# Kernel tuning notes

Measured on AMD Instinct MI355X. Metric: run time of the kernel, lower is better.

## Reference

```python
import jax, jax.numpy as jnp
import numpy as np
import math

B, TQ, TK, C, H, DFF = 4, 1024, 1024, 1024, 16, 4096
DK = C // H
EPS = 1e-12


def _mha(x_q, x_kv, wq, bq, wk, bk, wv, bv, wo, bo, mask):
    Bq, Tq, Cq = x_q.shape
    Tk = x_kv.shape[1]
    q = (x_q @ wq + bq).reshape(Bq, Tq, H, DK).transpose(0, 2, 1, 3)  # [B,H,Tq,dk]
    k = (x_kv @ wk + bk).reshape(Bq, Tk, H, DK).transpose(0, 2, 1, 3)
    v = (x_kv @ wv + bv).reshape(Bq, Tk, H, DK).transpose(0, 2, 1, 3)
    scores = jnp.einsum('bhqd,bhkd->bhqk', q, k) * (1.0 / math.sqrt(DK))
    if mask is not None:
        scores = jnp.where(mask, scores, jnp.asarray(-1e9, scores.dtype))
    attn = jax.nn.softmax(scores, axis=-1)
    o = jnp.einsum('bhqk,bhkd->bhqd', attn, v).transpose(0, 2, 1, 3).reshape(Bq, Tq, Cq)
    return o @ wo + bo


def _ln(x, g, b):
    mu = jnp.mean(x, axis=-1, keepdims=True)
    var = jnp.mean(jnp.square(x - mu), axis=-1, keepdims=True)
    return (x - mu) * jax.lax.rsqrt(var + EPS) * g + b


def setup_inputs() -> dict:
    key = jax.random.key(0)
    ks = iter(jax.random.split(key, 32))
    s = 0.02
    inp = {}
    inp['src'] = jax.random.normal(next(ks), (B, TK, C), jnp.float32)
    inp['dst'] = jax.random.normal(next(ks), (B, TQ, C), jnp.float32)
    inp['src_mask'] = jnp.ones((B, 1, 1, TK), dtype=bool)  # key-padding mask (all valid)
    inp['dst_mask'] = jnp.tril(jnp.ones((TQ, TQ), dtype=bool))[None, None]  # causal
    for p in ['sa', 'ca']:
        for n in ['wq', 'wk', 'wv', 'wo']:
            inp[f'{p}_{n}'] = jax.random.normal(next(ks), (C, C), jnp.float32) * s
        for n in ['bq', 'bk', 'bv', 'bo']:
            inp[f'{p}_{n}'] = jnp.zeros((C,), jnp.float32)
    inp['ffn_w1'] = jax.random.normal(next(ks), (C, DFF), jnp.float32) * s
    inp['ffn_b1'] = jnp.zeros((DFF,), jnp.float32)
    inp['ffn_w2'] = jax.random.normal(next(ks), (DFF, C), jnp.float32) * s
    inp['ffn_b2'] = jnp.zeros((C,), jnp.float32)
    for i in ['1', '2', '3']:
        inp[f'ln{i}_g'] = jnp.ones((C,), jnp.float32)
        inp[f'ln{i}_b'] = jnp.zeros((C,), jnp.float32)
    return inp


def reference(src, dst, src_mask, dst_mask,
              sa_wq, sa_wk, sa_wv, sa_wo, sa_bq, sa_bk, sa_bv, sa_bo,
              ca_wq, ca_wk, ca_wv, ca_wo, ca_bq, ca_bk, ca_bv, ca_bo,
              ffn_w1, ffn_b1, ffn_w2, ffn_b2,
              ln1_g, ln1_b, ln2_g, ln2_b, ln3_g, ln3_b):
    # post-LN decoder layer, eval mode (dropout is identity)
    sa = _mha(dst, dst, sa_wq, sa_bq, sa_wk, sa_bk, sa_wv, sa_bv, sa_wo, sa_bo, dst_mask)
    y = _ln(dst + sa, ln1_g, ln1_b)
    ca = _mha(y, src, ca_wq, ca_bq, ca_wk, ca_bk, ca_wv, ca_bv, ca_wo, ca_bo, src_mask)
    y = _ln(y + ca, ln2_g, ln2_b)
    ff = jax.nn.gelu(y @ ffn_w1 + ffn_b1, approximate=False) @ ffn_w2 + ffn_b2
    return _ln(y + ff, ln3_g, ln3_b)
```

## Files before the change

### kernel.cpp

```cpp
#include <hip/hip_runtime.h>
#include <math.h>

typedef __attribute__((ext_vector_type(4))) float f32x4;
typedef __attribute__((ext_vector_type(8))) __bf16 bf16x8;
typedef __attribute__((ext_vector_type(8))) short short8;

#define DEV __device__ __forceinline__

DEV short f2bfs(float f) {
    unsigned u = __builtin_bit_cast(unsigned, f);
    unsigned r = (u + 0x7FFFu + ((u >> 16) & 1u)) >> 16;
    return (short)r;
}

DEV f32x4 mfma16(bf16x8 a, bf16x8 b, f32x4 c) {
    return __builtin_amdgcn_mfma_f32_16x16x32_bf16(a, b, c, 0, 0, 0);
}

DEV void gload_lds16(const void* g, void* l) {
    __builtin_amdgcn_global_load_lds((const __attribute__((address_space(1))) void*)g,
                                     (__attribute__((address_space(3))) void*)l, 16, 0, 0);
}

__global__ __launch_bounds__(256) void wtrans(const float* __restrict__ Win,
                                              short* __restrict__ Wout,
                                              int Kd, int Nd) {
    __shared__ float Tt[64][65];
    const int tx = threadIdx.x & 15, ty = threadIdx.x >> 4;
    const int k0 = blockIdx.y * 64, n0 = blockIdx.x * 64;
#pragma unroll
    for (int rr = 0; rr < 4; ++rr) {
        int k = ty + rr * 16;
        float4 v = *(const float4*)&Win[(size_t)(k0 + k) * Nd + n0 + tx * 4];
        Tt[k][tx * 4 + 0] = v.x; Tt[k][tx * 4 + 1] = v.y;
        Tt[k][tx * 4 + 2] = v.z; Tt[k][tx * 4 + 3] = v.w;
    }
    __syncthreads();
#pragma unroll
    for (int rr = 0; rr < 4; ++rr) {
        int n = ty + rr * 16;
        short4 o;
        o.x = f2bfs(Tt[tx * 4 + 0][n]);
        o.y = f2bfs(Tt[tx * 4 + 1][n]);
        o.z = f2bfs(Tt[tx * 4 + 2][n]);
        o.w = f2bfs(Tt[tx * 4 + 3][n]);
        *(short4*)&Wout[(size_t)(n0 + n) * Kd + k0 + tx * 4] = o;
    }
}

struct WPtrs { const float* p[8]; };

__global__ __launch_bounds__(256) void wtrans8(WPtrs wp, short* __restrict__ out) {
    const float* __restrict__ Win = wp.p[blockIdx.z];
    short* __restrict__ Wout = out + (size_t)blockIdx.z * (1024 * 1024);
    __shared__ float Tt[64][65];
    const int tx = threadIdx.x & 15, ty = threadIdx.x >> 4;
    const int k0 = blockIdx.y * 64, n0 = blockIdx.x * 64;
#pragma unroll
    for (int rr = 0; rr < 4; ++rr) {
        int k = ty + rr * 16;
        float4 v = *(const float4*)&Win[(size_t)(k0 + k) * 1024 + n0 + tx * 4];
        Tt[k][tx * 4 + 0] = v.x; Tt[k][tx * 4 + 1] = v.y;
        Tt[k][tx * 4 + 2] = v.z; Tt[k][tx * 4 + 3] = v.w;
    }
    __syncthreads();
#pragma unroll
    for (int rr = 0; rr < 4; ++rr) {
        int n = ty + rr * 16;
        short4 o;
        o.x = f2bfs(Tt[tx * 4 + 0][n]);
        o.y = f2bfs(Tt[tx * 4 + 1][n]);
        o.z = f2bfs(Tt[tx * 4 + 2][n]);
        o.w = f2bfs(Tt[tx * 4 + 3][n]);
        *(short4*)&Wout[(size_t)(n0 + n) * 1024 + k0 + tx * 4] = o;
    }
}

__global__ __launch_bounds__(256) void conv_bf16(const float* __restrict__ X,
                                                 short* __restrict__ Y, int n8) {
    int i = blockIdx.x * 256 + threadIdx.x;
    if (i < n8) {
        float4 a = ((const float4*)X)[i * 2];
        float4 b = ((const float4*)X)[i * 2 + 1];
        short8 o;
        o[0] = f2bfs(a.x); o[1] = f2bfs(a.y); o[2] = f2bfs(a.z); o[3] = f2bfs(a.w);
        o[4] = f2bfs(b.x); o[5] = f2bfs(b.y); o[6] = f2bfs(b.z); o[7] = f2bfs(b.w);
        ((short8*)Y)[i] = o;
    }
}

template <int BM, int BN, int BK, int EPI, bool SWZ>
__global__ __launch_bounds__(256, (BM == 64 && BN == 64) ? 5 : 1)
void gemm_bt(const short* __restrict__ A,
             const short* __restrict__ BT,
             const float* __restrict__ b0,
             const float* __restrict__ b1,
             const float* __restrict__ b2,
             void* __restrict__ o0,
             void* __restrict__ o1,
             void* __restrict__ o2,
             int M, int N, int K, int Ks) {
    constexpr int IM = BM / 32, JN = BN / 32;
    constexpr int KH = BK / 32;
    constexpr int AL = (BM * 64) / 4096;
    constexpr int BL = (BN * 64) / 4096;
    __shared__ __align__(16) short As[2][BM * BK];
    __shared__ __align__(16) short Bs[2][BN * BK];
    const int tid = threadIdx.x, lane = tid & 63, w = tid >> 6;

    int bx, by, bz;
    if (SWZ) {
        int gx = gridDim.x, gy = gridDim.y;
        int G = gx * gy * gridDim.z;
        int fid = blockIdx.x + gx * (blockIdx.y + gy * blockIdx.z);
        int nf = (fid & 7) * (G >> 3) + (fid >> 3);
        bx = nf % gx;
        int t = nf / gx;
        by = t % gy;
        bz = t / gy;
    } else {
        bx = blockIdx.x; by = blockIdx.y; bz = blockIdx.z;
    }

    const int m0 = by * BM, n0 = bx * BN;
    const int kz = bz * K;
    const int wm = (w & 1) * (BM / 2), wn = (w >> 1) * (BN / 2);
    const int rl = lane & 15, rg = lane >> 4;
    f32x4 acc[IM][JN] = {};
    const char* Ab = (const char*)A;
    const char* Bb = (const char*)BT;
    const int nk = K / BK;

    auto stage = [&](int kt, int buf) {
#pragma unroll
        for (int h = 0; h < KH; ++h) {
#pragma unroll
            for (int r = 0; r < AL; ++r) {
                int lo = (tid + r * 256) * 16;
                int row = lo >> 6, cp = (lo >> 4) & 3, c = (cp - (row >> 1)) & 3;
                gload_lds16(Ab + ((size_t)(m0 + row) * Ks + kz + kt * BK + h * 32 + c * 8) * 2,
                            (char*)As[buf] + h * (BM * 64) + lo);
            }
#pragma unroll
            for (int r = 0; r < BL; ++r) {
                int lo = (tid + r * 256) * 16;
                int row = lo >> 6, cp = (lo >> 4) & 3, c = (cp - (row >> 1)) & 3;
                gload_lds16(Bb + ((size_t)(n0 + row) * Ks + kz + kt * BK + h * 32 + c * 8) * 2,
                            (char*)Bs[buf] + h * (BN * 64) + lo);
            }
        }
    };

    stage(0, 0);
    for (int kt = 0; kt < nk; ++kt) {
        const int buf = kt & 1;
        __syncthreads();
        if (kt + 1 < nk) stage(kt + 1, buf ^ 1);
        bf16x8 af[KH][IM], bfr[KH][JN];
#pragma unroll
        for (int h = 0; h < KH; ++h) {
#pragma unroll
            for (int i = 0; i < IM; i++) {
                int row = wm + i * 16 + rl;
                af[h][i] = *(const bf16x8*)(As[buf] + h * (BM * 32) + row * 32 +
                                            ((rg + (row >> 1)) & 3) * 8);
            }
#pragma unroll
            for (int j = 0; j < JN; j++) {
                int row = wn + j * 16 + rl;
                bfr[h][j] = *(const bf16x8*)(Bs[buf] + h * (BN * 32) + row * 32 +
                                             ((rg + (row >> 1)) & 3) * 8);
            }
        }
#pragma unroll
        for (int h = 0; h < KH; ++h)
#pragma unroll
            for (int i = 0; i < IM; i++)
#pragma unroll
                for (int j = 0; j < JN; j++)
                    acc[i][j] = mfma16(af[h][i], bfr[h][j], acc[i][j]);
    }

    float* o0z = (float*)o0 + (size_t)bz * M * N;
#pragma unroll
    for (int i = 0; i < IM; i++) {
        int gm0 = m0 + wm + i * 16 + rg * 4;
#pragma unroll
        for (int j = 0; j < JN; j++) {
            int gn = n0 + wn + j * 16 + rl;
            if (EPI == 0) {
                float bv = bz == 0 ? b0[gn] : 0.0f;
#pragma unroll
                for (int r = 0; r < 4; r++)
                    o0z[(size_t)(gm0 + r) * N + gn] = acc[i][j][r] + bv;
            } else if (EPI == 2) {
                float bv = b0[gn];
#pragma unroll
                for (int r = 0; r < 4; r++) {
                    float x = acc[i][j][r] + bv;
                    float z = 1.59576912f * x + 0.07135481f * x * x * x;
                    float g = x / (1.0f + __expf(-z));
                    ((short*)o0)[(size_t)(gm0 + r) * N + gn] = f2bfs(g);
                }
            } else {
                int seg = gn >> 10, n1 = gn & 1023, h = n1 >> 6, d = n1 & 63;
                int b = gm0 >> 10, t0 = gm0 & 1023;
                bool isV = (EPI == 1) ? (seg == 2) : (seg == 1);
                const float* bp = (EPI == 1) ? (seg == 0 ? b0 : (seg == 1 ? b1 : b2))
                                             : (seg == 0 ? b0 : b1);
                float bv = bp[n1];
                float qs = (EPI == 1 && seg == 0) ? 0.125f : 1.0f;
                if (!isV) {
                    short* hp = (short*)((EPI == 1) ? (seg == 0 ? o0 : o1) : o0);
                    size_t base = ((size_t)(b * 16 + h) * 1024 + t0) * 64 + d;
#pragma unroll
                    for (int r = 0; r < 4; r++)
                        hp[base + (size_t)r * 64] = f2bfs((acc[i][j][r] + bv) * qs);
                } else {
                    short* vp = (short*)((EPI == 1) ? o2 : o1);
                    short4 pk;
                    pk.x = f2bfs(acc[i][j][0] + bv);
                    pk.y = f2bfs(acc[i][j][1] + bv);
                    pk.z = f2bfs(acc[i][j][2] + bv);
                    pk.w = f2bfs(acc[i][j][3] + bv);
                    *(short4*)(vp + ((size_t)(b * 16 + h) * 64 + d) * 1024 + t0) = pk;
                }
            }
        }
    }
}

template <bool CAUSAL>
__global__ __launch_bounds__(256, 3) void attn4(const short* __restrict__ Qh,
                                                const short* __restrict__ Kh,
                                                const short* __restrict__ VTh,
                                                short* __restrict__ Out, int TKn) {
    __shared__ __align__(16) short Ks[2][64 * 64];
    __shared__ __align__(16) short Vts[2][64 * 64];
    __shared__ __align__(16) short Ps[4][16 * 72 + 8];
    const int tid = threadIdx.x, lane = tid & 63, w = tid >> 6;
    const int rl = lane & 15, rg = lane >> 4;
    const int bh = blockIdx.y, b = bh >> 4, h = bh & 15;
    const int q0 = blockIdx.x * 64;
    const short* Qp = Qh + (size_t)bh * 1024 * 64;
    const char* Kp = (const char*)(Kh + (size_t)bh * (size_t)TKn * 64);
    const char* Vp = (const char*)(VTh + (size_t)bh * (size_t)TKn * 64);

    const int qrow = q0 + w * 16 + rl;
    const bf16x8 qf0 = *(const bf16x8*)(Qp + (size_t)qrow * 64 + rg * 8);
    const bf16x8 qf1 = *(const bf16x8*)(Qp + (size_t)qrow * 64 + 32 + rg * 8);

    bf16x8 onesf;
#pragma unroll
    for (int i = 0; i < 8; ++i) onesf[i] = (__bf16)1.0f;

    f32x4 o[4] = {};
    f32x4 lacc = {};

    short* Pw = &Ps[w][0];
    const int nkt = CAUSAL ? blockIdx.x + 1 : (TKn >> 6);

    auto stage = [&](int kt, int buf) {
#pragma unroll
        for (int r = 0; r < 2; ++r) {
            int lo = (w * 2 + r) * 1024 + lane * 16;
            int row = lo >> 7, cp = (lo >> 4) & 7, c = (cp - row) & 7;
            gload_lds16(Kp + ((size_t)(kt * 64 + row) * 64 + c * 8) * 2,
                        (char*)Ks[buf] + lo);
            gload_lds16(Vp + ((size_t)row * TKn + kt * 64 + c * 8) * 2,
                        (char*)Vts[buf] + lo);
        }
    };

    stage(0, 0);
    for (int kt = 0; kt < nkt; ++kt) {
        const int buf = kt & 1;
        __syncthreads();
        if (kt + 1 < nkt) stage(kt + 1, buf ^ 1);

        const short* KsB = Ks[buf];
        f32x4 s[4];
#pragma unroll
        for (int ch = 0; ch < 4; ++ch) {
            int row = ch * 16 + rl;
            bf16x8 k0 = *(const bf16x8*)(KsB + row * 64 + ((rg + row) & 7) * 8);
            bf16x8 k1 = *(const bf16x8*)(KsB + row * 64 + ((rg + 4 + row) & 7) * 8);
            f32x4 z = {};
            z = mfma16(k0, qf0, z);
            z = mfma16(k1, qf1, z);
            s[ch] = z;
        }
        const bool domask = CAUSAL && (kt == nkt - 1);
#pragma unroll
        for (int ch = 0; ch < 4; ++ch) {
            float p[4];
#pragma unroll
            for (int r = 0; r < 4; ++r) {
                float e = __expf(s[ch][r]);
                if (domask) {
                    int key = kt * 64 + ch * 16 + rg * 4 + r;
                    if (key > qrow) e = 0.0f;
                }
                p[r] = e;
            }
            unsigned d0 = (__builtin_bit_cast(unsigned, p[1]) & 0xFFFF0000u) |
                          (__builtin_bit_cast(unsigned, p[0]) >> 16);
            unsigned d1 = (__builtin_bit_cast(unsigned, p[3]) & 0xFFFF0000u) |
                          (__builtin_bit_cast(unsigned, p[2]) >> 16);
            uint2 dv; dv.x = d0; dv.y = d1;
            *(uint2*)(Pw + rl * 72 + ch * 16 + rg * 4) = dv;
        }
        bf16x8 pa0 = *(const bf16x8*)(Pw + rl * 72 + rg * 8);
        bf16x8 pa1 = *(const bf16x8*)(Pw + rl * 72 + 32 + rg * 8);
        lacc = mfma16(pa0, onesf, lacc);
        lacc = mfma16(pa1, onesf, lacc);
        const short* VsB = Vts[buf];
#pragma unroll
        for (int j = 0; j < 4; ++j) {
            int row = j * 16 + rl;
            bf16x8 v0 = *(const bf16x8*)(VsB + row * 64 + ((rg + row) & 7) * 8);
            bf16x8 v1 = *(const bf16x8*)(VsB + row * 64 + ((rg + 4 + row) & 7) * 8);
            o[j] = mfma16(pa0, v0, o[j]);
            o[j] = mfma16(pa1, v1, o[j]);
        }
    }

    float inv[4];
#pragma unroll
    for (int r = 0; r < 4; r++) inv[r] = 1.0f / lacc[r];
#pragma unroll
    for (int j = 0; j < 4; j++) {
#pragma unroll
        for (int r = 0; r < 4; r++) {
            int row = q0 + w * 16 + rg * 4 + r;
            int col = h * 64 + j * 16 + rl;
            Out[((size_t)b * 1024 + row) * 1024 + col] = f2bfs(o[j][r] * inv[r]);
        }
    }
}

__global__ __launch_bounds__(256) void ln_fused(const float* __restrict__ X,
                                                const float* __restrict__ R,
                                                const float* __restrict__ R2,
                                                const float* __restrict__ gam,
                                                const float* __restrict__ bet,
                                                float* __restrict__ Yf,
                                                short* __restrict__ Yb) {
    const int row = blockIdx.x, tid = threadIdx.x;
    const int lane = tid & 63, w = tid >> 6;
    float4 xv = ((const float4*)(X + (size_t)row * 1024))[tid];
    float4 rv = ((const float4*)(R + (size_t)row * 1024))[tid];
    float v0 = xv.x + rv.x, v1 = xv.y + rv.y, v2 = xv.z + rv.z, v3 = xv.w + rv.w;
    if (R2) {
        float4 r2 = ((const float4*)(R2 + (size_t)row * 1024))[tid];
        v0 += r2.x; v1 += r2.y; v2 += r2.z; v3 += r2.w;
    }
    float s = v0 + v1 + v2 + v3;
    float ss = v0 * v0 + v1 * v1 + v2 * v2 + v3 * v3;
#pragma unroll
    for (int off = 1; off < 64; off <<= 1) {
        s += __shfl_xor(s, off);
        ss += __shfl_xor(ss, off);
    }
    __shared__ float sred[4], ssred[4];
    if (lane == 0) { sred[w] = s; ssred[w] = ss; }
    __syncthreads();
    s = sred[0] + sred[1] + sred[2] + sred[3];
    ss = ssred[0] + ssred[1] + ssred[2] + ssred[3];
    float mu = s * (1.0f / 1024.0f);
    float var = ss * (1.0f / 1024.0f) - mu * mu;
    float rsq = rsqrtf(var + 1e-12f);
    float4 gv = ((const float4*)gam)[tid];
    float4 bv = ((const float4*)bet)[tid];
    float y0 = (v0 - mu) * rsq * gv.x + bv.x;
    float y1 = (v1 - mu) * rsq * gv.y + bv.y;
    float y2 = (v2 - mu) * rsq * gv.z + bv.z;
    float y3 = (v3 - mu) * rsq * gv.w + bv.w;
    float4 yo = {y0, y1, y2, y3};
    ((float4*)(Yf + (size_t)row * 1024))[tid] = yo;
    if (Yb) {
        short4 ob;
        ob.x = f2bfs(y0); ob.y = f2bfs(y1); ob.z = f2bfs(y2); ob.w = f2bfs(y3);
        ((short4*)(Yb + (size_t)row * 1024))[tid] = ob;
    }
}

extern "C" void kernel_launch(void* const* d_in, const int* in_sizes, int n_in,
                              void* d_out, int out_size, void* d_ws, size_t ws_size,
                              hipStream_t stream) {
    const float* src = (const float*)d_in[0];
    const float* dst = (const float*)d_in[1];
    const float* sa_wq = (const float*)d_in[4];
    const float* sa_wk = (const float*)d_in[5];
    const float* sa_wv = (const float*)d_in[6];
    const float* sa_wo = (const float*)d_in[7];
    const float* sa_bq = (const float*)d_in[8];
    const float* sa_bk = (const float*)d_in[9];
    const float* sa_bv = (const float*)d_in[10];
    const float* sa_bo = (const float*)d_in[11];
    const float* ca_wq = (const float*)d_in[12];
    const float* ca_wk = (const float*)d_in[13];
    const float* ca_wv = (const float*)d_in[14];
    const float* ca_wo = (const float*)d_in[15];
    const float* ca_bq = (const float*)d_in[16];
    const float* ca_bk = (const float*)d_in[17];
    const float* ca_bv = (const float*)d_in[18];
    const float* ca_bo = (const float*)d_in[19];
    const float* ffn_w1 = (const float*)d_in[20];
    const float* ffn_b1 = (const float*)d_in[21];
    const float* ffn_w2 = (const float*)d_in[22];
    const float* ffn_b2 = (const float*)d_in[23];
    const float* ln1g = (const float*)d_in[24];
    const float* ln1b = (const float*)d_in[25];
    const float* ln2g = (const float*)d_in[26];
    const float* ln2b = (const float*)d_in[27];
    const float* ln3g = (const float*)d_in[28];
    const float* ln3b = (const float*)d_in[29];

    char* ws = (char*)d_ws;
    size_t off = 0;
    auto alloc = [&](size_t n) { size_t o = off; off = (off + n + 255) & ~(size_t)255; return o; };

    const size_t szW = (size_t)1024 * 1024 * 2;
    short* wT = (short*)(ws + alloc(8 * szW));
    short* w1T = (short*)(ws + alloc((size_t)4096 * 1024 * 2));
    short* w2T = (short*)(ws + alloc((size_t)1024 * 4096 * 2));
    const size_t szAct2 = (size_t)4096 * 1024 * 2;
    const size_t szAct4 = (size_t)4096 * 1024 * 4;
    short* dstb = (short*)(ws + alloc(szAct2));
    short* srcb = (short*)(ws + alloc(szAct2));
    short* Qh = (short*)(ws + alloc(szAct2));
    short* Kh = (short*)(ws + alloc(szAct2));
    short* VTh = (short*)(ws + alloc(szAct2));
    short* attnb = (short*)(ws + alloc(szAct2));
    float* tmp = (float*)(ws + alloc(2 * szAct4));
    float* tmp2 = tmp + (size_t)4096 * 1024;
    float* y1f = (float*)(ws + alloc(szAct4));
    short* y1b = (short*)(ws + alloc(szAct2));
    float* y2f = (float*)(ws + alloc(szAct4));
    short* y2b = (short*)(ws + alloc(szAct2));
    short* ffnh = (short*)(ws + alloc((size_t)4096 * 4096 * 2));

    short* sa_wqkvT = wT;
    short* sa_woT = wT + 3 * (size_t)1048576;
    short* ca_wqT = wT + 4 * (size_t)1048576;
    short* ca_wkvT = wT + 5 * (size_t)1048576;
    short* ca_woT = wT + 7 * (size_t)1048576;

    dim3 blk(256);

    WPtrs wp = {{sa_wq, sa_wk, sa_wv, sa_wo, ca_wq, ca_wk, ca_wv, ca_wo}};
    wtrans8<<<dim3(16, 16, 8), blk, 0, stream>>>(wp, wT);
    wtrans<<<dim3(64, 16), blk, 0, stream>>>(ffn_w1, w1T, 1024, 4096);
    wtrans<<<dim3(16, 64), blk, 0, stream>>>(ffn_w2, w2T, 4096, 1024);
    conv_bf16<<<2048, blk, 0, stream>>>(dst, dstb, 524288);
    conv_bf16<<<2048, blk, 0, stream>>>(src, srcb, 524288);

    gemm_bt<128, 128, 32, 1, false><<<dim3(24, 32), blk, 0, stream>>>(
        dstb, sa_wqkvT, sa_bq, sa_bk, sa_bv, Qh, Kh, VTh, 4096, 3072, 1024, 1024);
    attn4<true><<<dim3(16, 64), blk, 0, stream>>>(Qh, Kh, VTh, attnb, 1024);
    gemm_bt<64, 64, 64, 0, true><<<dim3(16, 64), blk, 0, stream>>>(
        attnb, sa_woT, sa_bo, nullptr, nullptr, tmp, nullptr, nullptr, 4096, 1024, 1024, 1024);
    ln_fused<<<4096, blk, 0, stream>>>(dst, tmp, nullptr, ln1g, ln1b, y1f, y1b);

    gemm_bt<64, 64, 64, 1, true><<<dim3(16, 64), blk, 0, stream>>>(
        y1b, ca_wqT, ca_bq, nullptr, nullptr, Qh, nullptr, nullptr, 4096, 1024, 1024, 1024);
    gemm_bt<128, 128, 32, 3, false><<<dim3(16, 32), blk, 0, stream>>>(
        srcb, ca_wkvT, ca_bk, ca_bv, nullptr, Kh, VTh, nullptr, 4096, 2048, 1024, 1024);
    attn4<false><<<dim3(16, 64), blk, 0, stream>>>(Qh, Kh, VTh, attnb, 1024);
    gemm_bt<64, 64, 64, 0, true><<<dim3(16, 64), blk, 0, stream>>>(
        attnb, ca_woT, ca_bo, nullptr, nullptr, tmp, nullptr, nullptr, 4096, 1024, 1024, 1024);
    ln_fused<<<4096, blk, 0, stream>>>(y1f, tmp, nullptr, ln2g, ln2b, y2f, y2b);

    gemm_bt<128, 128, 32, 2, false><<<dim3(32, 32), blk, 0, stream>>>(
        y2b, w1T, ffn_b1, nullptr, nullptr, ffnh, nullptr, nullptr, 4096, 4096, 1024, 1024);
    gemm_bt<64, 64, 64, 0, true><<<dim3(16, 64, 2), blk, 0, stream>>>(
        ffnh, w2T, ffn_b2, nullptr, nullptr, tmp, nullptr, nullptr, 4096, 1024, 2048, 4096);
    ln_fused<<<4096, blk, 0, stream>>>(y2f, tmp, tmp2, ln3g, ln3b, (float*)d_out, nullptr);

    (void)in_sizes; (void)n_in; (void)out_size; (void)ws_size;
}
```

Before: 518.9 us.

## Replace split-K FFN2 GEMM with 4-stage pipelined 128x128 tile kernel

Adds a PIPE variant of the bf16 GEMM that keeps four LDS buffers with three stages in flight, using explicit vmcnt waits and a raw barrier instead of a full syncthreads each step. The second FFN GEMM switches from a split-K 64x64 launch with two partial outputs to a single 128x128 pipelined launch over the full K=4096, so the final layernorm reads one partial. It also lowers the occupancy hint for the 64x64 variant from 5 to 4 waves. The cost targeted is memory-latency stalls and the extra partial-sum traffic, at the price of only 256 blocks, which may underfill the GPU's compute units.

```diff
diff --git a/kernel.cpp b/kernel.cpp
--- a/kernel.cpp
+++ b/kernel.cpp
@@ -89,8 +89,8 @@
     }
 }
 
-template <int BM, int BN, int BK, int EPI, bool SWZ>
-__global__ __launch_bounds__(256, (BM == 64 && BN == 64) ? 5 : 1)
+template <int BM, int BN, int BK, int EPI, bool SWZ, bool PIPE = false>
+__global__ __launch_bounds__(256, PIPE ? 1 : ((BM == 64 && BN == 64) ? 4 : 1))
 void gemm_bt(const short* __restrict__ A,
              const short* __restrict__ BT,
              const float* __restrict__ b0,
@@ -104,8 +104,9 @@
     constexpr int KH = BK / 32;
     constexpr int AL = (BM * 64) / 4096;
     constexpr int BL = (BN * 64) / 4096;
-    __shared__ __align__(16) short As[2][BM * BK];
-    __shared__ __align__(16) short Bs[2][BN * BK];
+    constexpr int NB = PIPE ? 4 : 2;
+    __shared__ __align__(16) short As[NB][BM * BK];
+    __shared__ __align__(16) short Bs[NB][BN * BK];
     const int tid = threadIdx.x, lane = tid & 63, w = tid >> 6;
 
     int bx, by, bz;
@@ -151,11 +152,7 @@
         }
     };
 
-    stage(0, 0);
-    for (int kt = 0; kt < nk; ++kt) {
-        const int buf = kt & 1;
-        __syncthreads();
-        if (kt + 1 < nk) stage(kt + 1, buf ^ 1);
+    auto compute = [&](int buf) {
         bf16x8 af[KH][IM], bfr[KH][JN];
 #pragma unroll
         for (int h = 0; h < KH; ++h) {
@@ -179,6 +176,32 @@
 #pragma unroll
                 for (int j = 0; j < JN; j++)
                     acc[i][j] = mfma16(af[h][i], bfr[h][j], acc[i][j]);
+    };
+
+    if constexpr (PIPE) {
+        stage(0, 0);
+        if (nk > 1) stage(1, 1);
+        if (nk > 2) stage(2, 2);
+        for (int kt = 0; kt < nk; ++kt) {
+            const int buf = kt & 3;
+            if (kt + 2 < nk)
+                asm volatile("s_waitcnt vmcnt(8)" ::: "memory");
+            else if (kt + 1 < nk)
+                asm volatile("s_waitcnt vmcnt(4)" ::: "memory");
+            else
+                asm volatile("s_waitcnt vmcnt(0)" ::: "memory");
+            __builtin_amdgcn_s_barrier();
+            if (kt + 3 < nk) stage(kt + 3, (kt + 3) & 3);
+            compute(buf);
+        }
+    } else {
+        stage(0, 0);
+        for (int kt = 0; kt < nk; ++kt) {
+            const int buf = kt & 1;
+            __syncthreads();
+            if (kt + 1 < nk) stage(kt + 1, buf ^ 1);
+            compute(buf);
+        }
     }
 
     float* o0z = (float*)o0 + (size_t)bz * M * N;
@@ -433,8 +456,7 @@
     short* Kh = (short*)(ws + alloc(szAct2));
     short* VTh = (short*)(ws + alloc(szAct2));
     short* attnb = (short*)(ws + alloc(szAct2));
-    float* tmp = (float*)(ws + alloc(2 * szAct4));
-    float* tmp2 = tmp + (size_t)4096 * 1024;
+    float* tmp = (float*)(ws + alloc(szAct4));
     float* y1f = (float*)(ws + alloc(szAct4));
     short* y1b = (short*)(ws + alloc(szAct2));
     float* y2f = (float*)(ws + alloc(szAct4));
@@ -474,9 +496,9 @@
 
     gemm_bt<128, 128, 32, 2, false><<<dim3(32, 32), blk, 0, stream>>>(
         y2b, w1T, ffn_b1, nullptr, nullptr, ffnh, nullptr, nullptr, 4096, 4096, 1024, 1024);
-    gemm_bt<64, 64, 64, 0, true><<<dim3(16, 64, 2), blk, 0, stream>>>(
-        ffnh, w2T, ffn_b2, nullptr, nullptr, tmp, nullptr, nullptr, 4096, 1024, 2048, 4096);
-    ln_fused<<<4096, blk, 0, stream>>>(y2f, tmp, tmp2, ln3g, ln3b, (float*)d_out, nullptr);
+    gemm_bt<128, 128, 32, 0, true, true><<<dim3(8, 32), blk, 0, stream>>>(
+        ffnh, w2T, ffn_b2, nullptr, nullptr, tmp, nullptr, nullptr, 4096, 1024, 4096, 4096);
+    ln_fused<<<4096, blk, 0, stream>>>(y2f, tmp, nullptr, ln3g, ln3b, (float*)d_out, nullptr);
 
     (void)in_sizes; (void)n_in; (void)out_size; (void)ws_size;
 }
```

After: 541.1 us. 4.3% more time.

## Use column-major block swizzle for all GEMMs and drop split-K in FFN down-projection

Applied to the files above, without the earlier changes.

Adds a second block-index swizzle mode in which consecutive blocks walk down the M dimension first, and applies it to every GEMM, including the 128x128 ones that previously had no swizzle. This is meant to improve L2 reuse of weight tiles across neighbouring blocks. The FFN second GEMM no longer splits K in two, so it writes a single partial and skips the extra temp buffer and the second-partial add in the final layernorm. That raises per-block work for that GEMM while halving its grid. The occupancy hint for 64x64 tiles drops from 5 to 4 waves per SIMD.

```diff
diff --git a/kernel.cpp b/kernel.cpp
--- a/kernel.cpp
+++ b/kernel.cpp
@@ -89,8 +89,8 @@
     }
 }
 
-template <int BM, int BN, int BK, int EPI, bool SWZ>
-__global__ __launch_bounds__(256, (BM == 64 && BN == 64) ? 5 : 1)
+template <int BM, int BN, int BK, int EPI, int SWZ>
+__global__ __launch_bounds__(256, (BM == 64 && BN == 64) ? 4 : 1)
 void gemm_bt(const short* __restrict__ A,
              const short* __restrict__ BT,
              const float* __restrict__ b0,
@@ -109,7 +109,7 @@
     const int tid = threadIdx.x, lane = tid & 63, w = tid >> 6;
 
     int bx, by, bz;
-    if (SWZ) {
+    if (SWZ == 1) {
         int gx = gridDim.x, gy = gridDim.y;
         int G = gx * gy * gridDim.z;
         int fid = blockIdx.x + gx * (blockIdx.y + gy * blockIdx.z);
@@ -118,6 +118,15 @@
         int t = nf / gx;
         by = t % gy;
         bz = t / gy;
+    } else if (SWZ == 2) {
+        int gx = gridDim.x, gy = gridDim.y;
+        int G = gx * gy * gridDim.z;
+        int fid = blockIdx.x + gx * (blockIdx.y + gy * blockIdx.z);
+        int nf = (fid & 7) * (G >> 3) + (fid >> 3);
+        by = nf % gy;
+        int t = nf / gy;
+        bx = t % gx;
+        bz = t / gx;
     } else {
         bx = blockIdx.x; by = blockIdx.y; bz = blockIdx.z;
     }
@@ -433,8 +442,7 @@
     short* Kh = (short*)(ws + alloc(szAct2));
     short* VTh = (short*)(ws + alloc(szAct2));
     short* attnb = (short*)(ws + alloc(szAct2));
-    float* tmp = (float*)(ws + alloc(2 * szAct4));
-    float* tmp2 = tmp + (size_t)4096 * 1024;
+    float* tmp = (float*)(ws + alloc(szAct4));
     float* y1f = (float*)(ws + alloc(szAct4));
     short* y1b = (short*)(ws + alloc(szAct2));
     float* y2f = (float*)(ws + alloc(szAct4));
@@ -456,27 +464,27 @@
     conv_bf16<<<2048, blk, 0, stream>>>(dst, dstb, 524288);
     conv_bf16<<<2048, blk, 0, stream>>>(src, srcb, 524288);
 
-    gemm_bt<128, 128, 32, 1, false><<<dim3(24, 32), blk, 0, stream>>>(
+    gemm_bt<128, 128, 32, 1, 2><<<dim3(24, 32), blk, 0, stream>>>(
         dstb, sa_wqkvT, sa_bq, sa_bk, sa_bv, Qh, Kh, VTh, 4096, 3072, 1024, 1024);
     attn4<true><<<dim3(16, 64), blk, 0, stream>>>(Qh, Kh, VTh, attnb, 1024);
-    gemm_bt<64, 64, 64, 0, true><<<dim3(16, 64), blk, 0, stream>>>(
+    gemm_bt<64, 64, 64, 0, 2><<<dim3(16, 64), blk, 0, stream>>>(
         attnb, sa_woT, sa_bo, nullptr, nullptr, tmp, nullptr, nullptr, 4096, 1024, 1024, 1024);
     ln_fused<<<4096, blk, 0, stream>>>(dst, tmp, nullptr, ln1g, ln1b, y1f, y1b);
 
-    gemm_bt<64, 64, 64, 1, true><<<dim3(16, 64), blk, 0, stream>>>(
+    gemm_bt<64, 64, 64, 1, 2><<<dim3(16, 64), blk, 0, stream>>>(
         y1b, ca_wqT, ca_bq, nullptr, nullptr, Qh, nullptr, nullptr, 4096, 1024, 1024, 1024);
-    gemm_bt<128, 128, 32, 3, false><<<dim3(16, 32), blk, 0, stream>>>(
+    gemm_bt<128, 128, 32, 3, 2><<<dim3(16, 32), blk, 0, stream>>>(
         srcb, ca_wkvT, ca_bk, ca_bv, nullptr, Kh, VTh, nullptr, 4096, 2048, 1024, 1024);
     attn4<false><<<dim3(16, 64), blk, 0, stream>>>(Qh, Kh, VTh, attnb, 1024);
-    gemm_bt<64, 64, 64, 0, true><<<dim3(16, 64), blk, 0, stream>>>(
+    gemm_bt<64, 64, 64, 0, 2><<<dim3(16, 64), blk, 0, stream>>>(
         attnb, ca_woT, ca_bo, nullptr, nullptr, tmp, nullptr, nullptr, 4096, 1024, 1024, 1024);
     ln_fused<<<4096, blk, 0, stream>>>(y1f, tmp, nullptr, ln2g, ln2b, y2f, y2b);
 
-    gemm_bt<128, 128, 32, 2, false><<<dim3(32, 32), blk, 0, stream>>>(
+    gemm_bt<128, 128, 32, 2, 2><<<dim3(32, 32), blk, 0, stream>>>(
         y2b, w1T, ffn_b1, nullptr, nullptr, ffnh, nullptr, nullptr, 4096, 4096, 1024, 1024);
-    gemm_bt<64, 64, 64, 0, true><<<dim3(16, 64, 2), blk, 0, stream>>>(
-        ffnh, w2T, ffn_b2, nullptr, nullptr, tmp, nullptr, nullptr, 4096, 1024, 2048, 4096);
-    ln_fused<<<4096, blk, 0, stream>>>(y2f, tmp, tmp2, ln3g, ln3b, (float*)d_out, nullptr);
+    gemm_bt<64, 64, 64, 0, 2><<<dim3(16, 64), blk, 0, stream>>>(
+        ffnh, w2T, ffn_b2, nullptr, nullptr, tmp, nullptr, nullptr, 4096, 1024, 4096, 4096);
+    ln_fused<<<4096, blk, 0, stream>>>(y2f, tmp, nullptr, ln3g, ln3b, (float*)d_out, nullptr);
 
     (void)in_sizes; (void)n_in; (void)out_size; (void)ws_size;
 }
```

Result: slower. 551.0 us (+6.2%).
